# Kernel optimization log

Hardware: AMD Instinct MI355X
Metric: run time of the kernel (lower is better)

The kernel has to match this reference:

```python
import jax, jax.numpy as jnp
import numpy as np

N, E, IN_DIM, OUT_DIM, EDGE_DIM = 50000, 800000, 256, 128, 64
NEG_SLOPE = 0.2


def setup_inputs() -> dict:
    key = jax.random.key(0)
    ks = jax.random.split(key, 8)
    xavier = lambda k, shape: jax.random.normal(k, shape, jnp.float32) * np.float32(np.sqrt(2.0 / (shape[0] + shape[1])))
    return {
        "nfeat": jax.random.normal(ks[0], (N, IN_DIM), jnp.float32),
        "ex": jax.random.normal(ks[1], (E, EDGE_DIM), jnp.float32),
        "src": jax.random.randint(ks[2], (E,), 0, N),
        "dst": jax.random.randint(ks[3], (E,), 0, N),
        "W_fc": xavier(ks[4], (OUT_DIM, IN_DIM)),
        "b_fc": jnp.zeros((OUT_DIM,), jnp.float32),
        "W_att": xavier(ks[5], (1, 2 * OUT_DIM + EDGE_DIM)),
        "b_att": jnp.zeros((1,), jnp.float32),
        "W_edge": xavier(ks[6], (OUT_DIM, EDGE_DIM)),
        "b_edge": jnp.zeros((OUT_DIM,), jnp.float32),
        "W_eatt": xavier(ks[7], (EDGE_DIM, EDGE_DIM)),
        "b_eatt": jnp.zeros((EDGE_DIM,), jnp.float32),
    }


def reference(nfeat, ex, src, dst, W_fc, b_fc, W_att, b_att, W_edge, b_edge, W_eatt, b_eatt):
    n = nfeat.shape[0]
    # node transform: z = fc(nfeat)  [N, OUT]
    z = nfeat @ W_fc.T + b_fc
    # edge transform for attention score calc  [E, EDGE_DIM]
    ex_t = ex @ W_eatt.T + b_eatt
    z_src = z[src]                                   # [E, OUT] gather
    # attention logits on concat[z_src, z_dst, ex_t]  [E, 1]
    z2 = jnp.concatenate([z_src, z[dst], ex_t], axis=1)
    e = jax.nn.leaky_relu(z2 @ W_att.T + b_att, NEG_SLOPE)
    # edge feature message  [E, OUT]
    ez = ex @ W_edge.T + b_edge
    # segment softmax over incoming edges of each dst node
    m = jax.ops.segment_max(e, dst, num_segments=n)  # [N, 1]
    w = jnp.exp(e - m[dst])
    denom = jax.ops.segment_sum(w, dst, num_segments=n)
    alpha = w / denom[dst]                           # [E, 1]
    # h = sum_e alpha * z_src + sum_e alpha * ez (apply_attention_on_edge)
    h = jax.ops.segment_sum(alpha * (z_src + ez), dst, num_segments=n)  # [N, OUT]
    return h, alpha
```

## Files before the change

kernel.cpp:

```cpp
#include <hip/hip_runtime.h>
#include <math.h>
#include <float.h>

#define IN_D 256
#define OUT_D 128
#define ED_D 64
#define NEG 0.2f

typedef __attribute__((ext_vector_type(8))) short bf16x8;
typedef __attribute__((ext_vector_type(4))) float f32x4;

__device__ __forceinline__ unsigned short f2bf(float f) {
    unsigned u = __float_as_uint(f);
    unsigned r = (u + 0x7FFFu + ((u >> 16) & 1u)) >> 16;
    return (unsigned short)r;
}

__global__ __launch_bounds__(256) void k_init(
        const float* __restrict__ W_att, const float* __restrict__ b_att,
        const float* __restrict__ W_eatt, const float* __restrict__ b_eatt,
        const float* __restrict__ W_fc, const float* __restrict__ W_edge,
        float* __restrict__ u, float* __restrict__ c0,
        unsigned short* __restrict__ Wb, float2* __restrict__ Wt2,
        int* __restrict__ cnt, int* __restrict__ fill, int N) {
    int idx = blockIdx.x * 256 + threadIdx.x;
    if (idx < N) { cnt[idx] = 0; fill[idx] = 0; }
    if (idx < IN_D * OUT_D) {
        int i = idx & 7;
        int lane = (idx >> 3) & 63;
        int rest = idx >> 9;
        int nt = rest & 7, ks = rest >> 3;
        int col = nt * 16 + (lane & 15);
        int k = ks * 32 + (lane >> 4) * 8 + i;
        Wb[idx] = f2bf(W_fc[col * IN_D + k]);
    }
    if (idx < ED_D * (OUT_D / 2)) {
        int k = idx >> 6, l = idx & 63;
        Wt2[idx] = make_float2(W_edge[(2 * l) * ED_D + k], W_edge[(2 * l + 1) * ED_D + k]);
    }
    if (idx < ED_D) {
        float acc = 0.f;
        for (int j = 0; j < ED_D; ++j) acc += W_att[256 + j] * W_eatt[j * ED_D + idx];
        u[idx] = acc;
    }
    if (idx == ED_D) {
        float c = 0.f;
        for (int j = 0; j < ED_D; ++j) c += W_att[256 + j] * b_eatt[j];
        c0[0] = c + b_att[0];
    }
}

__global__ __launch_bounds__(256) void k_hist(const int* __restrict__ dst,
                                              int* __restrict__ cnt, int E) {
    int i = blockIdx.x * 256 + threadIdx.x;
    if (i < E) atomicAdd(&cnt[dst[i]], 1);
}

#define LDA 272
__global__ __launch_bounds__(256) void k_node(
        const float* __restrict__ nfeat, const unsigned short* __restrict__ Wb,
        const float* __restrict__ b_fc, const float* __restrict__ W_att,
        float* __restrict__ z, float* __restrict__ asrc, float* __restrict__ adst, int n) {
    __shared__ unsigned short sa[128 * LDA];
    int t = threadIdx.x;
    int row_base = blockIdx.x * 128;

    int r8 = t >> 3, c8 = t & 7;
#pragma unroll
    for (int p = 0; p < 4; ++p) {
        int r = p * 32 + r8;
        int node = row_base + r; if (node >= n) node = n - 1;
        const float4* srcp = (const float4*)(nfeat + (size_t)node * IN_D);
#pragma unroll
        for (int q = 0; q < 8; ++q) {
            int c4 = q * 8 + c8;
            float4 v = srcp[c4];
            unsigned pk0 = (unsigned)f2bf(v.x) | ((unsigned)f2bf(v.y) << 16);
            unsigned pk1 = (unsigned)f2bf(v.z) | ((unsigned)f2bf(v.w) << 16);
            *(uint2*)&sa[(size_t)r * LDA + c4 * 4] = make_uint2(pk0, pk1);
        }
    }
    __syncthreads();

    int lane = t & 63, w = t >> 6;
    int lr = lane & 15, lg = lane >> 4;

    f32x4 acc[2][8];
#pragma unroll
    for (int mi = 0; mi < 2; ++mi)
#pragma unroll
        for (int nt = 0; nt < 8; ++nt) acc[mi][nt] = (f32x4)(0.f);

    const bf16x8* wb8 = (const bf16x8*)Wb;
#pragma unroll
    for (int ks = 0; ks < 8; ++ks) {
        bf16x8 af[2], bfr[8];
#pragma unroll
        for (int mi = 0; mi < 2; ++mi) {
            int row = (2 * w + mi) * 16 + lr;
            af[mi] = *(const bf16x8*)&sa[(size_t)row * LDA + ks * 32 + lg * 8];
        }
#pragma unroll
        for (int nt = 0; nt < 8; ++nt)
            bfr[nt] = wb8[(ks * 8 + nt) * 64 + lane];
#pragma unroll
        for (int mi = 0; mi < 2; ++mi)
#pragma unroll
            for (int nt = 0; nt < 8; ++nt)
                acc[mi][nt] = __builtin_amdgcn_mfma_f32_16x16x32_bf16(
                    af[mi], bfr[nt], acc[mi][nt], 0, 0, 0);
    }

    float w1c[8], w2c[8], bfc[8];
#pragma unroll
    for (int nt = 0; nt < 8; ++nt) {
        int col = nt * 16 + lr;
        w1c[nt] = W_att[col];
        w2c[nt] = W_att[128 + col];
        bfc[nt] = b_fc[col];
    }
#pragma unroll
    for (int mi = 0; mi < 2; ++mi) {
        float p1[4] = {0.f, 0.f, 0.f, 0.f}, p2[4] = {0.f, 0.f, 0.f, 0.f};
#pragma unroll
        for (int nt = 0; nt < 8; ++nt) {
#pragma unroll
            for (int reg = 0; reg < 4; ++reg) {
                float zv = acc[mi][nt][reg] + bfc[nt];
                int m = row_base + (2 * w + mi) * 16 + lg * 4 + reg;
                if (m < n) z[(size_t)m * OUT_D + nt * 16 + lr] = zv;
                p1[reg] = fmaf(zv, w1c[nt], p1[reg]);
                p2[reg] = fmaf(zv, w2c[nt], p2[reg]);
            }
        }
#pragma unroll
        for (int reg = 0; reg < 4; ++reg) {
#pragma unroll
            for (int off = 1; off <= 8; off <<= 1) {
                p1[reg] += __shfl_xor(p1[reg], off);
                p2[reg] += __shfl_xor(p2[reg], off);
            }
        }
        if (lr == 0) {
#pragma unroll
            for (int reg = 0; reg < 4; ++reg) {
                int m = row_base + (2 * w + mi) * 16 + lg * 4 + reg;
                if (m < n) { asrc[m] = p1[reg]; adst[m] = p2[reg]; }
            }
        }
    }
}

__global__ __launch_bounds__(1024) void k_scan(const int* __restrict__ cnt,
                                               int* __restrict__ rowptr, int N) {
    int t = threadIdx.x;
    int per = (N + 1023) / 1024;
    int b0 = t * per, b1 = b0 + per;
    if (b0 > N) b0 = N;
    if (b1 > N) b1 = N;
    int s = 0;
    for (int i = b0; i < b1; ++i) s += cnt[i];
    int wl = t & 63, w = t >> 6;
    int v = s;
#pragma unroll
    for (int off = 1; off < 64; off <<= 1) {
        int a = __shfl_up(v, off);
        if (wl >= off) v += a;
    }
    __shared__ int wsum[16], woff[16];
    if (wl == 63) wsum[w] = v;
    __syncthreads();
    if (t == 0) { int r = 0; for (int i = 0; i < 16; ++i) { woff[i] = r; r += wsum[i]; } }
    __syncthreads();
    int run = woff[w] + v - s;
    for (int i = b0; i < b1; ++i) { rowptr[i] = run; run += cnt[i]; }
    if (t == 1023) rowptr[N] = run;
}

__global__ __launch_bounds__(256) void k_edge(
        const float* __restrict__ ex, const int* __restrict__ src, const int* __restrict__ dst,
        const float* __restrict__ asrc, const float* __restrict__ adst,
        const float* __restrict__ u, const float* __restrict__ c0,
        const int* __restrict__ rowptr, int* __restrict__ fill,
        int4* __restrict__ csr, int E) {
    int i = blockIdx.x * 256 + threadIdx.x;
    if (i >= E) return;
    const float4* exr = (const float4*)(ex + (size_t)i * ED_D);
    const float4* u4 = (const float4*)u;
    float acc = 0.f;
#pragma unroll
    for (int q = 0; q < 16; ++q) {
        float4 a = exr[q], b = u4[q];
        acc += a.x * b.x + a.y * b.y + a.z * b.z + a.w * b.w;
    }
    int s = src[i], d = dst[i];
    float e = acc + asrc[s] + adst[d] + c0[0];
    e = (e > 0.f) ? e : NEG * e;
    int pos = rowptr[d] + atomicAdd(&fill[d], 1);
    csr[pos] = make_int4(__float_as_int(e), i, s, 0);
}

__global__ __launch_bounds__(256) void k_gather(
        const float4* __restrict__ zf4, const float2* __restrict__ ex2,
        const int4* __restrict__ csr, const int* __restrict__ rowptr,
        float4* __restrict__ h4, float* __restrict__ alpha_out,
        float2* __restrict__ xsum2, int N) {
    int lane = threadIdx.x & 63;
    int half = lane >> 5, hl = lane & 31;
    int n = blockIdx.x * 4 + (threadIdx.x >> 6);
    if (n >= N) return;
    int beg = rowptr[n], end = rowptr[n + 1];
    int deg = end - beg;
    if (deg == 0) return;
    float4 accz = make_float4(0.f, 0.f, 0.f, 0.f);
    float2 accx = make_float2(0.f, 0.f);

    if (deg <= 64) {
        int4 me = make_int4(0, 0, 0, 0);
        float lg = -FLT_MAX;
        if (lane < deg) { me = csr[beg + lane]; lg = __int_as_float(me.x); }
        float m = lg;
#pragma unroll
        for (int off = 32; off >= 1; off >>= 1) m = fmaxf(m, __shfl_xor(m, off));
        float wvv = (lane < deg) ? expf(lg - m) : 0.f;
        float sw = wvv;
#pragma unroll
        for (int off = 32; off >= 1; off >>= 1) sw += __shfl_xor(sw, off);
        float al = wvv / sw;
        if (lane < deg) alpha_out[me.y] = al;
        int j = 0;
        for (; j + 8 <= deg; j += 8) {
            float a[4]; int s[4], e[4];
#pragma unroll
            for (int q = 0; q < 4; ++q) {
                int idx = j + 2 * q + half;
                a[q] = __shfl(al, idx);
                s[q] = __shfl(me.z, idx);
                e[q] = __shfl(me.y, idx);
            }
            float4 zv[4]; float2 xv[4];
#pragma unroll
            for (int q = 0; q < 4; ++q) {
                zv[q] = zf4[(size_t)s[q] * 32 + hl];
                xv[q] = ex2[(size_t)e[q] * 32 + hl];
            }
#pragma unroll
            for (int q = 0; q < 4; ++q) {
                accz.x = fmaf(a[q], zv[q].x, accz.x);
                accz.y = fmaf(a[q], zv[q].y, accz.y);
                accz.z = fmaf(a[q], zv[q].z, accz.z);
                accz.w = fmaf(a[q], zv[q].w, accz.w);
                accx.x = fmaf(a[q], xv[q].x, accx.x);
                accx.y = fmaf(a[q], xv[q].y, accx.y);
            }
        }
        for (; j < deg; j += 2) {
            int idx = j + half;
            float a = __shfl(al, idx);
            int s = __shfl(me.z, idx), e = __shfl(me.y, idx);
            float4 zv = zf4[(size_t)s * 32 + hl];
            float2 xv = ex2[(size_t)e * 32 + hl];
            accz.x = fmaf(a, zv.x, accz.x);
            accz.y = fmaf(a, zv.y, accz.y);
            accz.z = fmaf(a, zv.z, accz.z);
            accz.w = fmaf(a, zv.w, accz.w);
            accx.x = fmaf(a, xv.x, accx.x);
            accx.y = fmaf(a, xv.y, accx.y);
        }
    } else {
        float m = -FLT_MAX;
        for (int c = beg + lane; c < end; c += 64)
            m = fmaxf(m, __int_as_float(csr[c].x));
#pragma unroll
        for (int off = 32; off >= 1; off >>= 1) m = fmaxf(m, __shfl_xor(m, off));
        float sw = 0.f;
        for (int c = beg + lane; c < end; c += 64)
            sw += expf(__int_as_float(csr[c].x) - m);
#pragma unroll
        for (int off = 32; off >= 1; off >>= 1) sw += __shfl_xor(sw, off);
        float rden = 1.f / sw;
        for (int c = beg; c < end; c += 64) {
            int mcnt = end - c;
            if (mcnt > 64) mcnt = 64;
            int4 me = make_int4(0, 0, 0, 0);
            float al = 0.f;
            if (lane < mcnt) {
                me = csr[c + lane];
                al = expf(__int_as_float(me.x) - m) * rden;
                alpha_out[me.y] = al;
            }
            int j = 0;
            for (; j + 8 <= mcnt; j += 8) {
                float a[4]; int s[4], e[4];
#pragma unroll
                for (int q = 0; q < 4; ++q) {
                    int idx = j + 2 * q + half;
                    a[q] = __shfl(al, idx);
                    s[q] = __shfl(me.z, idx);
                    e[q] = __shfl(me.y, idx);
                }
                float4 zv[4]; float2 xv[4];
#pragma unroll
                for (int q = 0; q < 4; ++q) {
                    zv[q] = zf4[(size_t)s[q] * 32 + hl];
                    xv[q] = ex2[(size_t)e[q] * 32 + hl];
                }
#pragma unroll
                for (int q = 0; q < 4; ++q) {
                    accz.x = fmaf(a[q], zv[q].x, accz.x);
                    accz.y = fmaf(a[q], zv[q].y, accz.y);
                    accz.z = fmaf(a[q], zv[q].z, accz.z);
                    accz.w = fmaf(a[q], zv[q].w, accz.w);
                    accx.x = fmaf(a[q], xv[q].x, accx.x);
                    accx.y = fmaf(a[q], xv[q].y, accx.y);
                }
            }
            for (; j < mcnt; j += 2) {
                int idx = j + half;
                float a = __shfl(al, idx);
                int s = __shfl(me.z, idx), e = __shfl(me.y, idx);
                float4 zv = zf4[(size_t)s * 32 + hl];
                float2 xv = ex2[(size_t)e * 32 + hl];
                accz.x = fmaf(a, zv.x, accz.x);
                accz.y = fmaf(a, zv.y, accz.y);
                accz.z = fmaf(a, zv.z, accz.z);
                accz.w = fmaf(a, zv.w, accz.w);
                accx.x = fmaf(a, xv.x, accx.x);
                accx.y = fmaf(a, xv.y, accx.y);
            }
        }
    }
    accz.x += __shfl_xor(accz.x, 32);
    accz.y += __shfl_xor(accz.y, 32);
    accz.z += __shfl_xor(accz.z, 32);
    accz.w += __shfl_xor(accz.w, 32);
    accx.x += __shfl_xor(accx.x, 32);
    accx.y += __shfl_xor(accx.y, 32);
    if (half == 0) {
        h4[(size_t)n * 32 + hl] = accz;
        xsum2[(size_t)n * 32 + hl] = accx;
    }
}

__global__ __launch_bounds__(256) void k_xmm(
        const float2* __restrict__ Wt2, const float* __restrict__ b_edge,
        const float* __restrict__ xsum, const int* __restrict__ rowptr,
        float2* __restrict__ h2, int N) {
    __shared__ float2 swt[ED_D * 64];
    for (int i = threadIdx.x; i < ED_D * 64; i += 256) swt[i] = Wt2[i];
    __syncthreads();
    int lane = threadIdx.x & 63;
    int wv = threadIdx.x >> 6;
    float2 be2 = ((const float2*)b_edge)[lane];
    for (int n = blockIdx.x * 4 + wv; n < N; n += gridDim.x * 4) {
        int deg = rowptr[n + 1] - rowptr[n];
        if (deg == 0) {
            h2[(size_t)n * 64 + lane] = make_float2(0.f, 0.f);
            continue;
        }
        float xk = xsum[(size_t)n * 64 + lane];
        float2 hv = h2[(size_t)n * 64 + lane];
        hv.x += be2.x; hv.y += be2.y;
#pragma unroll 8
        for (int k = 0; k < 64; ++k) {
            float a = __shfl(xk, k);
            float2 w2 = swt[k * 64 + lane];
            hv.x = fmaf(a, w2.x, hv.x);
            hv.y = fmaf(a, w2.y, hv.y);
        }
        h2[(size_t)n * 64 + lane] = hv;
    }
}

extern "C" void kernel_launch(void* const* d_in, const int* in_sizes, int n_in,
                              void* d_out, int out_size, void* d_ws, size_t ws_size,
                              hipStream_t stream) {
    const float* nfeat = (const float*)d_in[0];
    const float* ex    = (const float*)d_in[1];
    const int*   src   = (const int*)d_in[2];
    const int*   dst   = (const int*)d_in[3];
    const float* W_fc  = (const float*)d_in[4];
    const float* b_fc  = (const float*)d_in[5];
    const float* W_att = (const float*)d_in[6];
    const float* b_att = (const float*)d_in[7];
    const float* W_edge = (const float*)d_in[8];
    const float* b_edge = (const float*)d_in[9];
    const float* W_eatt = (const float*)d_in[10];
    const float* b_eatt = (const float*)d_in[11];
    int N = in_sizes[0] / IN_D;
    int E = in_sizes[2];

    float* h_out = (float*)d_out;
    float* alpha_out = h_out + (size_t)N * OUT_D;

    char* w = (char*)d_ws;
    auto alloc = [&](size_t bytes) { char* p = w; w += (bytes + 255) & ~255ull; return p; };
    float* z      = (float*)alloc((size_t)N * OUT_D * 4);
    float* asrc   = (float*)alloc((size_t)N * 4);
    float* adst   = (float*)alloc((size_t)N * 4);
    int* cnt      = (int*)alloc((size_t)N * 4);
    int* rowptr   = (int*)alloc(((size_t)N + 1) * 4);
    int* fill     = (int*)alloc((size_t)N * 4);
    int4* csr     = (int4*)alloc((size_t)E * 16);
    float* xsum   = (float*)alloc((size_t)N * ED_D * 4);
    unsigned short* Wb = (unsigned short*)alloc((size_t)IN_D * OUT_D * 2);
    float2* Wt2   = (float2*)alloc((size_t)ED_D * 64 * 8);
    float* u      = (float*)alloc(64 * 4);
    float* c0     = (float*)alloc(4);

    int init_total = N > IN_D * OUT_D ? N : IN_D * OUT_D;
    k_init<<<(init_total + 255) / 256, 256, 0, stream>>>(
        W_att, b_att, W_eatt, b_eatt, W_fc, W_edge, u, c0, Wb, Wt2, cnt, fill, N);
    k_hist<<<(E + 255) / 256, 256, 0, stream>>>(dst, cnt, E);
    k_node<<<(N + 127) / 128, 256, 0, stream>>>(nfeat, Wb, b_fc, W_att, z, asrc, adst, N);
    k_scan<<<1, 1024, 0, stream>>>(cnt, rowptr, N);
    k_edge<<<(E + 255) / 256, 256, 0, stream>>>(ex, src, dst, asrc, adst, u, c0,
                                                rowptr, fill, csr, E);
    k_gather<<<(N + 3) / 4, 256, 0, stream>>>((const float4*)z, (const float2*)ex, csr, rowptr,
                                              (float4*)h_out, alpha_out, (float2*)xsum, N);
    k_xmm<<<(N + 3) / 4, 256, 0, stream>>>((const float2*)Wt2, b_edge, xsum, rowptr,
                                           (float2*)h_out, N);
}
```

Measured before the change: 428.0 us.

## Reuse histogram atomic ranks for CSR placement and shrink CSR entries to int2

The histogram kernel now records each edge's atomic return value as its rank, so the edge kernel places entries at rowptr+rank. This removes the second pass of atomics on a fill array and the zeroing of that array. CSR entries shrink from int4 to int2 (logit, edge id), and the gather kernel instead loads src[edge id] per lane. The gather also gets a 4-edge remainder step before the 2-edge tail. The cost is an extra E-sized rank array write and read, plus a dependent indirect load of src in the gather.

```diff
diff --git a/kernel.cpp b/kernel.cpp
--- a/kernel.cpp
+++ b/kernel.cpp
@@ -22,9 +22,9 @@
         const float* __restrict__ W_fc, const float* __restrict__ W_edge,
         float* __restrict__ u, float* __restrict__ c0,
         unsigned short* __restrict__ Wb, float2* __restrict__ Wt2,
-        int* __restrict__ cnt, int* __restrict__ fill, int N) {
+        int* __restrict__ cnt, int N) {
     int idx = blockIdx.x * 256 + threadIdx.x;
-    if (idx < N) { cnt[idx] = 0; fill[idx] = 0; }
+    if (idx < N) cnt[idx] = 0;
     if (idx < IN_D * OUT_D) {
         int i = idx & 7;
         int lane = (idx >> 3) & 63;
@@ -51,9 +51,10 @@
 }
 
 __global__ __launch_bounds__(256) void k_hist(const int* __restrict__ dst,
-                                              int* __restrict__ cnt, int E) {
+                                              int* __restrict__ cnt,
+                                              int* __restrict__ rank, int E) {
     int i = blockIdx.x * 256 + threadIdx.x;
-    if (i < E) atomicAdd(&cnt[dst[i]], 1);
+    if (i < E) rank[i] = atomicAdd(&cnt[dst[i]], 1);
 }
 
 #define LDA 272
@@ -181,8 +182,8 @@
         const float* __restrict__ ex, const int* __restrict__ src, const int* __restrict__ dst,
         const float* __restrict__ asrc, const float* __restrict__ adst,
         const float* __restrict__ u, const float* __restrict__ c0,
-        const int* __restrict__ rowptr, int* __restrict__ fill,
-        int4* __restrict__ csr, int E) {
+        const int* __restrict__ rowptr, const int* __restrict__ rank,
+        int2* __restrict__ csr, int E) {
     int i = blockIdx.x * 256 + threadIdx.x;
     if (i >= E) return;
     const float4* exr = (const float4*)(ex + (size_t)i * ED_D);
@@ -196,13 +197,14 @@
     int s = src[i], d = dst[i];
     float e = acc + asrc[s] + adst[d] + c0[0];
     e = (e > 0.f) ? e : NEG * e;
-    int pos = rowptr[d] + atomicAdd(&fill[d], 1);
-    csr[pos] = make_int4(__float_as_int(e), i, s, 0);
+    int pos = rowptr[d] + rank[i];
+    csr[pos] = make_int2(__float_as_int(e), i);
 }
 
 __global__ __launch_bounds__(256) void k_gather(
         const float4* __restrict__ zf4, const float2* __restrict__ ex2,
-        const int4* __restrict__ csr, const int* __restrict__ rowptr,
+        const int* __restrict__ srcv, const int2* __restrict__ csr,
+        const int* __restrict__ rowptr,
         float4* __restrict__ h4, float* __restrict__ alpha_out,
         float2* __restrict__ xsum2, int N) {
     int lane = threadIdx.x & 63;
@@ -216,9 +218,14 @@
     float2 accx = make_float2(0.f, 0.f);
 
     if (deg <= 64) {
-        int4 me = make_int4(0, 0, 0, 0);
+        int2 me = make_int2(0, 0);
+        int sl = 0;
         float lg = -FLT_MAX;
-        if (lane < deg) { me = csr[beg + lane]; lg = __int_as_float(me.x); }
+        if (lane < deg) {
+            me = csr[beg + lane];
+            lg = __int_as_float(me.x);
+            sl = srcv[me.y];
+        }
         float m = lg;
 #pragma unroll
         for (int off = 32; off >= 1; off >>= 1) m = fmaxf(m, __shfl_xor(m, off));
@@ -235,7 +242,7 @@
             for (int q = 0; q < 4; ++q) {
                 int idx = j + 2 * q + half;
                 a[q] = __shfl(al, idx);
-                s[q] = __shfl(me.z, idx);
+                s[q] = __shfl(sl, idx);
                 e[q] = __shfl(me.y, idx);
             }
             float4 zv[4]; float2 xv[4];
@@ -254,10 +261,36 @@
                 accx.y = fmaf(a[q], xv[q].y, accx.y);
             }
         }
+        if (j + 4 <= deg) {
+            float a[2]; int s[2], e[2];
+#pragma unroll
+            for (int q = 0; q < 2; ++q) {
+                int idx = j + 2 * q + half;
+                a[q] = __shfl(al, idx);
+                s[q] = __shfl(sl, idx);
+                e[q] = __shfl(me.y, idx);
+            }
+            float4 zv[2]; float2 xv[2];
+#pragma unroll
+            for (int q = 0; q < 2; ++q) {
+                zv[q] = zf4[(size_t)s[q] * 32 + hl];
+                xv[q] = ex2[(size_t)e[q] * 32 + hl];
+            }
+#pragma unroll
+            for (int q = 0; q < 2; ++q) {
+                accz.x = fmaf(a[q], zv[q].x, accz.x);
+                accz.y = fmaf(a[q], zv[q].y, accz.y);
+                accz.z = fmaf(a[q], zv[q].z, accz.z);
+                accz.w = fmaf(a[q], zv[q].w, accz.w);
+                accx.x = fmaf(a[q], xv[q].x, accx.x);
+                accx.y = fmaf(a[q], xv[q].y, accx.y);
+            }
+            j += 4;
+        }
         for (; j < deg; j += 2) {
             int idx = j + half;
             float a = __shfl(al, idx);
-            int s = __shfl(me.z, idx), e = __shfl(me.y, idx);
+            int s = __shfl(sl, idx), e = __shfl(me.y, idx);
             float4 zv = zf4[(size_t)s * 32 + hl];
             float2 xv = ex2[(size_t)e * 32 + hl];
             accz.x = fmaf(a, zv.x, accz.x);
@@ -282,12 +315,14 @@
         for (int c = beg; c < end; c += 64) {
             int mcnt = end - c;
             if (mcnt > 64) mcnt = 64;
-            int4 me = make_int4(0, 0, 0, 0);
+            int2 me = make_int2(0, 0);
+            int sl = 0;
             float al = 0.f;
             if (lane < mcnt) {
                 me = csr[c + lane];
                 al = expf(__int_as_float(me.x) - m) * rden;
                 alpha_out[me.y] = al;
+                sl = srcv[me.y];
             }
             int j = 0;
             for (; j + 8 <= mcnt; j += 8) {
@@ -296,7 +331,7 @@
                 for (int q = 0; q < 4; ++q) {
                     int idx = j + 2 * q + half;
                     a[q] = __shfl(al, idx);
-                    s[q] = __shfl(me.z, idx);
+                    s[q] = __shfl(sl, idx);
                     e[q] = __shfl(me.y, idx);
                 }
                 float4 zv[4]; float2 xv[4];
@@ -318,7 +353,7 @@
             for (; j < mcnt; j += 2) {
                 int idx = j + half;
                 float a = __shfl(al, idx);
-                int s = __shfl(me.z, idx), e = __shfl(me.y, idx);
+                int s = __shfl(sl, idx), e = __shfl(me.y, idx);
                 float4 zv = zf4[(size_t)s * 32 + hl];
                 float2 xv = ex2[(size_t)e * 32 + hl];
                 accz.x = fmaf(a, zv.x, accz.x);
@@ -400,8 +435,8 @@
     float* adst   = (float*)alloc((size_t)N * 4);
     int* cnt      = (int*)alloc((size_t)N * 4);
     int* rowptr   = (int*)alloc(((size_t)N + 1) * 4);
-    int* fill     = (int*)alloc((size_t)N * 4);
-    int4* csr     = (int4*)alloc((size_t)E * 16);
+    int* rank     = (int*)alloc((size_t)E * 4);
+    int2* csr     = (int2*)alloc((size_t)E * 8);
     float* xsum   = (float*)alloc((size_t)N * ED_D * 4);
     unsigned short* Wb = (unsigned short*)alloc((size_t)IN_D * OUT_D * 2);
     float2* Wt2   = (float2*)alloc((size_t)ED_D * 64 * 8);
@@ -410,14 +445,15 @@
 
     int init_total = N > IN_D * OUT_D ? N : IN_D * OUT_D;
     k_init<<<(init_total + 255) / 256, 256, 0, stream>>>(
-        W_att, b_att, W_eatt, b_eatt, W_fc, W_edge, u, c0, Wb, Wt2, cnt, fill, N);
-    k_hist<<<(E + 255) / 256, 256, 0, stream>>>(dst, cnt, E);
+        W_att, b_att, W_eatt, b_eatt, W_fc, W_edge, u, c0, Wb, Wt2, cnt, N);
+    k_hist<<<(E + 255) / 256, 256, 0, stream>>>(dst, cnt, rank, E);
     k_node<<<(N + 127) / 128, 256, 0, stream>>>(nfeat, Wb, b_fc, W_att, z, asrc, adst, N);
     k_scan<<<1, 1024, 0, stream>>>(cnt, rowptr, N);
     k_edge<<<(E + 255) / 256, 256, 0, stream>>>(ex, src, dst, asrc, adst, u, c0,
-                                                rowptr, fill, csr, E);
-    k_gather<<<(N + 3) / 4, 256, 0, stream>>>((const float4*)z, (const float2*)ex, csr, rowptr,
-                                              (float4*)h_out, alpha_out, (float2*)xsum, N);
+                                                rowptr, rank, csr, E);
+    k_gather<<<(N + 3) / 4, 256, 0, stream>>>((const float4*)z, (const float2*)ex, src, csr,
+                                              rowptr, (float4*)h_out, alpha_out,
+                                              (float2*)xsum, N);
     k_xmm<<<(N + 3) / 4, 256, 0, stream>>>((const float2*)Wt2, b_edge, xsum, rowptr,
                                            (float2*)h_out, N);
 }
```

After: 411.2 us. 3.9% less time.
